# Kernel tuning notes

Hardware: AMD Instinct MI355X
Metric: run time of the kernel (lower is better)

Reference implementation:

```python
import jax, jax.numpy as jnp
import numpy as np


def setup_inputs() -> dict:
    key = jax.random.key(0)
    k_x, k_b = jax.random.split(key)
    B, C, H, W = 32, 512, 32, 32
    x = jax.random.normal(k_x, (B, C, H, W), dtype=jnp.float32)
    beta = jax.random.normal(k_b, (1,), dtype=jnp.float32)
    return {"x": x, "beta": beta}


def reference(x, beta):
    B, C, H, W = x.shape
    feat = x.reshape(B, C, H * W)                       # [B, C, N]
    # channel-channel Gram matrix: [B, C, C]
    attn = jnp.einsum('bcn,bdn->bcd', feat, feat)
    # DANet-style reversed scores: rowmax - score, then softmax over last dim
    attn = jnp.max(attn, axis=-1, keepdims=True) - attn
    attn = jax.nn.softmax(attn, axis=-1)
    feat_e = jnp.einsum('bcd,bdn->bcn', attn, feat).reshape(B, C, H, W)
    return beta * feat_e + x
```

## Files before the change

### kernel.cpp

```cpp
#include <hip/hip_runtime.h>
#include <math.h>

constexpr int B = 32, C = 512, N = 1024;

typedef float f32x4 __attribute__((ext_vector_type(4)));
typedef _Float16 f16x8 __attribute__((ext_vector_type(8)));
typedef unsigned short u16x4 __attribute__((ext_vector_type(4)));
typedef unsigned short u16x8 __attribute__((ext_vector_type(8)));

__device__ __forceinline__ unsigned short f32_to_f16u(float v) {
  union { _Float16 h; unsigned short u; } cv; cv.h = (_Float16)v; return cv.u;
}
__device__ __forceinline__ float f16u_to_f32(unsigned short u) {
  union { _Float16 h; unsigned short u; } cv; cv.u = u; return (float)cv.h;
}

__device__ __forceinline__ void glds16(const void* g, void* l) {
  __builtin_amdgcn_global_load_lds((const __attribute__((address_space(1))) void*)g,
                                   (__attribute__((address_space(3))) void*)l, 16, 0, 0);
}

__global__ __launch_bounds__(256) void convert_kernel(const float* __restrict__ x,
                                                      unsigned short* __restrict__ xf,
                                                      unsigned short* __restrict__ xfT) {
  const int b = blockIdx.z;
  const int cy = blockIdx.y * 64;
  const int nx = blockIdx.x * 64;
  const int t = threadIdx.x;
  const int r = t >> 4, c4 = (t & 15) * 4;

  __shared__ unsigned T[64][65];

#pragma unroll
  for (int rr = 0; rr < 64; rr += 16) {
    const int row = rr + r;
    const size_t gi = ((size_t)b * C + cy + row) * N + nx + c4;
    const float4 v = *(const float4*)&x[gi];
    u16x4 h;
    h[0] = f32_to_f16u(v.x); h[1] = f32_to_f16u(v.y);
    h[2] = f32_to_f16u(v.z); h[3] = f32_to_f16u(v.w);
    *(u16x4*)&xf[gi] = h;
    T[row][c4 + 0] = h[0]; T[row][c4 + 1] = h[1];
    T[row][c4 + 2] = h[2]; T[row][c4 + 3] = h[3];
  }
  __syncthreads();
#pragma unroll
  for (int rr = 0; rr < 64; rr += 16) {
    const int nrow = rr + r;
    u16x4 o;
    o[0] = (unsigned short)T[c4 + 0][nrow]; o[1] = (unsigned short)T[c4 + 1][nrow];
    o[2] = (unsigned short)T[c4 + 2][nrow]; o[3] = (unsigned short)T[c4 + 3][nrow];
    *(u16x4*)&xfT[((size_t)b * N + nx + nrow) * C + cy + c4] = o;
  }
}

__global__ __launch_bounds__(512, 2) void gram_soft_av(const unsigned short* __restrict__ xf,
                                                       const unsigned short* __restrict__ xfT,
                                                       const float* __restrict__ beta,
                                                       float* __restrict__ out) {
  const int l = blockIdx.x;
  const int xcd = l & 7, seq = l >> 3;
  const int b = xcd + 8 * (seq >> 3);
  const int i0 = (seq & 7) * 64;

  const unsigned short* __restrict__ Fh = xf  + (size_t)b * C * N;
  const unsigned short* __restrict__ FT = xfT + (size_t)b * N * C;
  float* __restrict__ ob = out + (size_t)b * C * N;

  __shared__ __align__(16) unsigned short Pb[4][512 * 32];
  unsigned short* Atile = &Pb[2][0];

  const int t = threadIdx.x, wave = t >> 6, lane = t & 63;
  const int lrow = lane & 15, quad = lane >> 4;
  const int srow = lane >> 2;
  const int sel  = ((lane & 3) ^ ((lane >> 3) & 3)) * 8;

  f32x4 acc[4][4] = {};

#define STAGE1(k0, nb)                                                    \
  {                                                                       \
    _Pragma("unroll")                                                     \
    for (int cc = 0; cc < 4; ++cc) {                                      \
      const int chunk = wave * 4 + cc;                                    \
      const int row = chunk * 16 + srow;                                  \
      glds16(Fh + (size_t)row * N + (k0) + sel, &Pb[nb][chunk * 512]);    \
    }                                                                     \
  }

#define LOADFRAG1(AH, BH, jj)                                             \
  {                                                                       \
    const unsigned short* __restrict__ Pc = Pb[(jj) & 3];                 \
    _Pragma("unroll")                                                     \
    for (int ti = 0; ti < 4; ++ti) {                                      \
      const int r = i0 + ti * 16 + lrow;                                  \
      AH[ti] = *(const f16x8*)&Pc[r * 32 + (quad ^ ((r >> 1) & 3)) * 8];  \
    }                                                                     \
    _Pragma("unroll")                                                     \
    for (int tj = 0; tj < 4; ++tj) {                                      \
      const int r = wave * 64 + tj * 16 + lrow;                           \
      BH[tj] = *(const f16x8*)&Pc[r * 32 + (quad ^ ((r >> 1) & 3)) * 8];  \
    }                                                                     \
  }

#define MFMA16(AH, BH, ACC)                                               \
  {                                                                       \
    __builtin_amdgcn_s_setprio(1);                                        \
    _Pragma("unroll")                                                     \
    for (int ti = 0; ti < 4; ++ti)                                        \
      _Pragma("unroll")                                                   \
      for (int tj = 0; tj < 4; ++tj)                                      \
        ACC[ti][tj] = __builtin_amdgcn_mfma_f32_16x16x32_f16(AH[ti], BH[tj], ACC[ti][tj], 0, 0, 0); \
    __builtin_amdgcn_s_setprio(0);                                        \
  }

#define P1BODY(CA, CB, NA, NB, j)                                         \
  {                                                                       \
    if ((j) < 29)       asm volatile("s_waitcnt vmcnt(8) lgkmcnt(0)" ::: "memory"); \
    else if ((j) == 29) asm volatile("s_waitcnt vmcnt(4) lgkmcnt(0)" ::: "memory"); \
    else                asm volatile("s_waitcnt vmcnt(0) lgkmcnt(0)" ::: "memory"); \
    __builtin_amdgcn_s_barrier();                                         \
    if ((j) + 4 < 32) STAGE1(((j) + 4) * 32, ((j) + 4) & 3);              \
    if ((j) + 1 < 32) LOADFRAG1(NA, NB, (j) + 1);                         \
    MFMA16(CA, CB, acc);                                                  \
  }

  STAGE1(0, 0);
  STAGE1(32, 1);
  STAGE1(64, 2);
  STAGE1(96, 3);
  asm volatile("s_waitcnt vmcnt(12)" ::: "memory");
  __builtin_amdgcn_s_barrier();

  f16x8 a0h[4], b0h[4], a1h[4], b1h[4];
  LOADFRAG1(a0h, b0h, 0);

  for (int j = 0; j < 32; j += 2) {
    P1BODY(a0h, b0h, a1h, b1h, j);
    P1BODY(a1h, b1h, a0h, b0h, j + 1);
  }
#undef P1BODY
#undef STAGE1

  __syncthreads();
  float* red = (float*)&Pb[0][0];
  float* fin = red + 512;

  float m[16];
#pragma unroll
  for (int ti = 0; ti < 4; ++ti)
#pragma unroll
    for (int rr = 0; rr < 4; ++rr)
      m[ti * 4 + rr] = fminf(fminf(acc[ti][0][rr], acc[ti][1][rr]),
                             fminf(acc[ti][2][rr], acc[ti][3][rr]));
#pragma unroll
  for (int o = 1; o < 16; o <<= 1)
#pragma unroll
    for (int s = 0; s < 16; ++s) m[s] = fminf(m[s], __shfl_xor(m[s], o, 64));
  if (lrow == 0)
#pragma unroll
    for (int ti = 0; ti < 4; ++ti)
#pragma unroll
      for (int rr = 0; rr < 4; ++rr)
        red[wave * 64 + ti * 16 + quad * 4 + rr] = m[ti * 4 + rr];
  __syncthreads();
  if (t < 64) {
    float v = red[t];
#pragma unroll
    for (int j = 1; j < 8; ++j) v = fminf(v, red[j * 64 + t]);
    fin[t] = v;
  }
  __syncthreads();

  float sm[16];
#pragma unroll
  for (int ti = 0; ti < 4; ++ti)
#pragma unroll
    for (int rr = 0; rr < 4; ++rr) {
      const float mn = fin[ti * 16 + quad * 4 + rr];
      float s = 0.f;
#pragma unroll
      for (int tj = 0; tj < 4; ++tj) {
        const float e = __expf(mn - acc[ti][tj][rr]);
        acc[ti][tj][rr] = e;
        s += e;
      }
      sm[ti * 4 + rr] = s;
    }
#pragma unroll
  for (int o = 1; o < 16; o <<= 1)
#pragma unroll
    for (int s = 0; s < 16; ++s) sm[s] += __shfl_xor(sm[s], o, 64);
  if (lrow == 0)
#pragma unroll
    for (int ti = 0; ti < 4; ++ti)
#pragma unroll
      for (int rr = 0; rr < 4; ++rr)
        red[wave * 64 + ti * 16 + quad * 4 + rr] = sm[ti * 4 + rr];
  __syncthreads();
  if (t < 64) {
    float v = 0.f;
#pragma unroll
    for (int j = 0; j < 8; ++j) v += red[j * 64 + t];
    fin[t] = 1.0f / v;
  }
  __syncthreads();

#pragma unroll
  for (int ti = 0; ti < 4; ++ti)
#pragma unroll
    for (int rr = 0; rr < 4; ++rr) {
      const float inv = fin[ti * 16 + quad * 4 + rr];
      const int rl = ti * 16 + quad * 4 + rr;
#pragma unroll
      for (int tj = 0; tj < 4; ++tj) {
        const int gcol = wave * 64 + tj * 16 + lrow;
        Atile[rl * 512 + ((((gcol >> 3) ^ (rl & 7)) << 3) | (gcol & 7))] =
            f32_to_f16u(acc[ti][tj][rr] * inv);
      }
    }
  __syncthreads();

  const float bv = beta[0];

  for (int jp = 0; jp < 2; ++jp) {
    f32x4 eacc[4][4] = {};
    u16x8 rsA[4];
#define LOADR_E(k0)                                                            \
    {                                                                          \
      _Pragma("unroll")                                                        \
      for (int cc = 0; cc < 4; ++cc) {                                         \
        const int chunk = wave * 4 + cc;                                       \
        const int row = chunk * 16 + srow;                                     \
        rsA[cc] = *(const u16x8*)&FT[(size_t)(jp * 512 + row) * C + (k0) + sel]; \
      }                                                                        \
    }
#define WRITER_E(nb)                                                           \
    {                                                                          \
      _Pragma("unroll")                                                        \
      for (int cc = 0; cc < 4; ++cc) {                                         \
        const int chunk = wave * 4 + cc;                                       \
        *(u16x8*)&Pb[nb][chunk * 512 + lane * 8] = rsA[cc];                    \
      }                                                                        \
    }
#define LOADFRAG2(AH, BH, uu)                                                  \
    {                                                                          \
      const unsigned short* __restrict__ Pc = Pb[(uu) & 1];                    \
      const int kk = (uu) * 32;                                                \
      _Pragma("unroll")                                                        \
      for (int ti = 0; ti < 4; ++ti) {                                         \
        const int ra = ti * 16 + lrow;                                         \
        AH[ti] = *(const f16x8*)&Atile[ra * 512 + ((((kk >> 3) + quad) ^ (ra & 7)) << 3)]; \
      }                                                                        \
      _Pragma("unroll")                                                        \
      for (int tj = 0; tj < 4; ++tj) {                                         \
        const int rb = wave * 64 + tj * 16 + lrow;                             \
        BH[tj] = *(const f16x8*)&Pc[rb * 32 + ((quad ^ ((rb >> 1) & 3)) << 3)]; \
      }                                                                        \
    }
#define P2BODY(CA, CB, NA, NB, u)                                              \
    {                                                                          \
      if ((u) + 1 < 16) WRITER_E(((u) + 1) & 1);                               \
      if ((u) + 2 < 16) LOADR_E(((u) + 2) * 32);                               \
      asm volatile("s_waitcnt lgkmcnt(0)" ::: "memory");                       \
      __builtin_amdgcn_s_barrier();                                            \
      if ((u) + 1 < 16) LOADFRAG2(NA, NB, (u) + 1);                            \
      MFMA16(CA, CB, eacc);                                                    \
    }

    LOADR_E(0);
    WRITER_E(0);
    LOADR_E(32);
    asm volatile("s_waitcnt lgkmcnt(0)" ::: "memory");
    __builtin_amdgcn_s_barrier();
    LOADFRAG2(a0h, b0h, 0);

    for (int u = 0; u < 16; u += 2) {
      P2BODY(a0h, b0h, a1h, b1h, u);
      P2BODY(a1h, b1h, a0h, b0h, u + 1);
    }
#undef P2BODY
#undef LOADFRAG2
#undef LOADR_E
#undef WRITER_E

    float* fs = (float*)&Pb[0][0] + wave * 1024;
#pragma unroll
    for (int ti = 0; ti < 4; ++ti) {
#pragma unroll
      for (int tj = 0; tj < 4; ++tj)
#pragma unroll
        for (int r = 0; r < 4; ++r)
          fs[(quad * 4 + r) * 64 + tj * 16 + lrow] = eacc[ti][tj][r];
      asm volatile("s_waitcnt lgkmcnt(0)" ::: "memory");
#pragma unroll
      for (int p = 0; p < 4; ++p) {
        const int f = p * 64 + lane;
        const int rr2 = f >> 4, cc4 = (f & 15) * 4;
        const f32x4 e = *(const f32x4*)&fs[rr2 * 64 + cc4];
        const int gr = i0 + ti * 16 + rr2;
        const int gc = jp * 512 + wave * 64 + cc4;
        const size_t o = (size_t)gr * N + gc;
        const u16x4 xv = *(const u16x4*)&Fh[o];
        f32x4 ov;
        ov[0] = fmaf(bv, e[0], f16u_to_f32(xv[0]));
        ov[1] = fmaf(bv, e[1], f16u_to_f32(xv[1]));
        ov[2] = fmaf(bv, e[2], f16u_to_f32(xv[2]));
        ov[3] = fmaf(bv, e[3], f16u_to_f32(xv[3]));
        __builtin_nontemporal_store(ov, (f32x4*)&ob[o]);
      }
      asm volatile("s_waitcnt lgkmcnt(0)" ::: "memory");
    }
  }
#undef MFMA16
#undef LOADFRAG1
}

extern "C" void kernel_launch(void* const* d_in, const int* in_sizes, int n_in,
                              void* d_out, int out_size, void* d_ws, size_t ws_size,
                              hipStream_t stream) {
  const float* x    = (const float*)d_in[0];
  const float* beta = (const float*)d_in[1];
  float* out = (float*)d_out;

  char* ws = (char*)d_ws;
  unsigned short* xf  = (unsigned short*)ws; ws += (size_t)B * C * N * 2;
  unsigned short* xfT = (unsigned short*)ws;

  convert_kernel<<<dim3(N / 64, C / 64, B), dim3(256), 0, stream>>>(x, xf, xfT);
  gram_soft_av  <<<dim3(256),               dim3(512), 0, stream>>>(xf, xfT, beta, out);
}
```

Baseline: 171.0 us.

## Load MFMA operands directly from global memory instead of LDS staging

Drops the LDS-staged, barrier-synchronised pipelines in both the Gram and attention-times-V phases. Each wave now loads its f16 fragments straight from global memory (xf and xfT) into registers, double-buffering them in registers across MFMA steps. This removes barriers, LDS traffic and the async global-to-LDS copies, but it issues redundant global loads across waves and uncoalesced 16-byte row reads, leaning on L2/L1 instead of shared memory. The LDS buffers are split into separate static arrays as a side effect.

```diff
diff --git a/kernel.cpp b/kernel.cpp
--- a/kernel.cpp
+++ b/kernel.cpp
@@ -6,18 +6,12 @@
 typedef float f32x4 __attribute__((ext_vector_type(4)));
 typedef _Float16 f16x8 __attribute__((ext_vector_type(8)));
 typedef unsigned short u16x4 __attribute__((ext_vector_type(4)));
-typedef unsigned short u16x8 __attribute__((ext_vector_type(8)));
 
 __device__ __forceinline__ unsigned short f32_to_f16u(float v) {
   union { _Float16 h; unsigned short u; } cv; cv.h = (_Float16)v; return cv.u;
 }
 __device__ __forceinline__ float f16u_to_f32(unsigned short u) {
   union { _Float16 h; unsigned short u; } cv; cv.u = u; return (float)cv.h;
-}
-
-__device__ __forceinline__ void glds16(const void* g, void* l) {
-  __builtin_amdgcn_global_load_lds((const __attribute__((address_space(1))) void*)g,
-                                   (__attribute__((address_space(3))) void*)l, 16, 0, 0);
 }
 
 __global__ __launch_bounds__(256) void convert_kernel(const float* __restrict__ x,
@@ -59,48 +53,23 @@
                                                        const float* __restrict__ beta,
                                                        float* __restrict__ out) {
   const int l = blockIdx.x;
-  const int xcd = l & 7, seq = l >> 3;
-  const int b = xcd + 8 * (seq >> 3);
+  const int seq = l >> 3;
+  const int b = (l & 7) + 8 * (seq >> 3);
   const int i0 = (seq & 7) * 64;
 
   const unsigned short* __restrict__ Fh = xf  + (size_t)b * C * N;
   const unsigned short* __restrict__ FT = xfT + (size_t)b * N * C;
   float* __restrict__ ob = out + (size_t)b * C * N;
 
-  __shared__ __align__(16) unsigned short Pb[4][512 * 32];
-  unsigned short* Atile = &Pb[2][0];
+  __shared__ __align__(16) unsigned short Atile[64 * 512];
+  __shared__ float red[512];
+  __shared__ float fin[64];
+  __shared__ __align__(16) float fsA[8][1024];
 
   const int t = threadIdx.x, wave = t >> 6, lane = t & 63;
   const int lrow = lane & 15, quad = lane >> 4;
-  const int srow = lane >> 2;
-  const int sel  = ((lane & 3) ^ ((lane >> 3) & 3)) * 8;
 
   f32x4 acc[4][4] = {};
-
-#define STAGE1(k0, nb)                                                    \
-  {                                                                       \
-    _Pragma("unroll")                                                     \
-    for (int cc = 0; cc < 4; ++cc) {                                      \
-      const int chunk = wave * 4 + cc;                                    \
-      const int row = chunk * 16 + srow;                                  \
-      glds16(Fh + (size_t)row * N + (k0) + sel, &Pb[nb][chunk * 512]);    \
-    }                                                                     \
-  }
-
-#define LOADFRAG1(AH, BH, jj)                                             \
-  {                                                                       \
-    const unsigned short* __restrict__ Pc = Pb[(jj) & 3];                 \
-    _Pragma("unroll")                                                     \
-    for (int ti = 0; ti < 4; ++ti) {                                      \
-      const int r = i0 + ti * 16 + lrow;                                  \
-      AH[ti] = *(const f16x8*)&Pc[r * 32 + (quad ^ ((r >> 1) & 3)) * 8];  \
-    }                                                                     \
-    _Pragma("unroll")                                                     \
-    for (int tj = 0; tj < 4; ++tj) {                                      \
-      const int r = wave * 64 + tj * 16 + lrow;                           \
-      BH[tj] = *(const f16x8*)&Pc[r * 32 + (quad ^ ((r >> 1) & 3)) * 8];  \
-    }                                                                     \
-  }
 
 #define MFMA16(AH, BH, ACC)                                               \
   {                                                                       \
@@ -113,37 +82,27 @@
     __builtin_amdgcn_s_setprio(0);                                        \
   }
 
-#define P1BODY(CA, CB, NA, NB, j)                                         \
+#define LDG1(AH, BH, j)                                                   \
   {                                                                       \
-    if ((j) < 29)       asm volatile("s_waitcnt vmcnt(8) lgkmcnt(0)" ::: "memory"); \
-    else if ((j) == 29) asm volatile("s_waitcnt vmcnt(4) lgkmcnt(0)" ::: "memory"); \
-    else                asm volatile("s_waitcnt vmcnt(0) lgkmcnt(0)" ::: "memory"); \
-    __builtin_amdgcn_s_barrier();                                         \
-    if ((j) + 4 < 32) STAGE1(((j) + 4) * 32, ((j) + 4) & 3);              \
-    if ((j) + 1 < 32) LOADFRAG1(NA, NB, (j) + 1);                         \
-    MFMA16(CA, CB, acc);                                                  \
-  }
-
-  STAGE1(0, 0);
-  STAGE1(32, 1);
-  STAGE1(64, 2);
-  STAGE1(96, 3);
-  asm volatile("s_waitcnt vmcnt(12)" ::: "memory");
-  __builtin_amdgcn_s_barrier();
-
-  f16x8 a0h[4], b0h[4], a1h[4], b1h[4];
-  LOADFRAG1(a0h, b0h, 0);
-
+    const int k0 = (j) * 32 + quad * 8;                                   \
+    _Pragma("unroll")                                                     \
+    for (int ti = 0; ti < 4; ++ti)                                        \
+      AH[ti] = *(const f16x8*)&Fh[(size_t)(i0 + ti * 16 + lrow) * N + k0];\
+    _Pragma("unroll")                                                     \
+    for (int tj = 0; tj < 4; ++tj)                                        \
+      BH[tj] = *(const f16x8*)&Fh[(size_t)(wave * 64 + tj * 16 + lrow) * N + k0]; \
+  }
+
+  f16x8 a0[4], b0[4], a1[4], b1[4];
+  LDG1(a0, b0, 0);
+  LDG1(a1, b1, 1);
   for (int j = 0; j < 32; j += 2) {
-    P1BODY(a0h, b0h, a1h, b1h, j);
-    P1BODY(a1h, b1h, a0h, b0h, j + 1);
-  }
-#undef P1BODY
-#undef STAGE1
-
-  __syncthreads();
-  float* red = (float*)&Pb[0][0];
-  float* fin = red + 512;
+    MFMA16(a0, b0, acc);
+    if (j + 2 < 32) LDG1(a0, b0, j + 2);
+    MFMA16(a1, b1, acc);
+    if (j + 3 < 32) LDG1(a1, b1, j + 3);
+  }
+#undef LDG1
 
   float m[16];
 #pragma unroll
@@ -224,66 +183,30 @@
 
   for (int jp = 0; jp < 2; ++jp) {
     f32x4 eacc[4][4] = {};
-    u16x8 rsA[4];
-#define LOADR_E(k0)                                                            \
+#define LDG2(AH, BH, u)                                                        \
     {                                                                          \
-      _Pragma("unroll")                                                        \
-      for (int cc = 0; cc < 4; ++cc) {                                         \
-        const int chunk = wave * 4 + cc;                                       \
-        const int row = chunk * 16 + srow;                                     \
-        rsA[cc] = *(const u16x8*)&FT[(size_t)(jp * 512 + row) * C + (k0) + sel]; \
-      }                                                                        \
-    }
-#define WRITER_E(nb)                                                           \
-    {                                                                          \
-      _Pragma("unroll")                                                        \
-      for (int cc = 0; cc < 4; ++cc) {                                         \
-        const int chunk = wave * 4 + cc;                                       \
-        *(u16x8*)&Pb[nb][chunk * 512 + lane * 8] = rsA[cc];                    \
-      }                                                                        \
-    }
-#define LOADFRAG2(AH, BH, uu)                                                  \
-    {                                                                          \
-      const unsigned short* __restrict__ Pc = Pb[(uu) & 1];                    \
-      const int kk = (uu) * 32;                                                \
+      const int kk = (u) * 32;                                                 \
       _Pragma("unroll")                                                        \
       for (int ti = 0; ti < 4; ++ti) {                                         \
         const int ra = ti * 16 + lrow;                                         \
         AH[ti] = *(const f16x8*)&Atile[ra * 512 + ((((kk >> 3) + quad) ^ (ra & 7)) << 3)]; \
       }                                                                        \
       _Pragma("unroll")                                                        \
-      for (int tj = 0; tj < 4; ++tj) {                                         \
-        const int rb = wave * 64 + tj * 16 + lrow;                             \
-        BH[tj] = *(const f16x8*)&Pc[rb * 32 + ((quad ^ ((rb >> 1) & 3)) << 3)]; \
-      }                                                                        \
-    }
-#define P2BODY(CA, CB, NA, NB, u)                                              \
-    {                                                                          \
-      if ((u) + 1 < 16) WRITER_E(((u) + 1) & 1);                               \
-      if ((u) + 2 < 16) LOADR_E(((u) + 2) * 32);                               \
-      asm volatile("s_waitcnt lgkmcnt(0)" ::: "memory");                       \
-      __builtin_amdgcn_s_barrier();                                            \
-      if ((u) + 1 < 16) LOADFRAG2(NA, NB, (u) + 1);                            \
-      MFMA16(CA, CB, eacc);                                                    \
-    }
-
-    LOADR_E(0);
-    WRITER_E(0);
-    LOADR_E(32);
-    asm volatile("s_waitcnt lgkmcnt(0)" ::: "memory");
-    __builtin_amdgcn_s_barrier();
-    LOADFRAG2(a0h, b0h, 0);
-
+      for (int tj = 0; tj < 4; ++tj)                                           \
+        BH[tj] = *(const f16x8*)&FT[(size_t)(jp * 512 + wave * 64 + tj * 16 + lrow) * C + kk + quad * 8]; \
+    }
+
+    LDG2(a0, b0, 0);
+    LDG2(a1, b1, 1);
     for (int u = 0; u < 16; u += 2) {
-      P2BODY(a0h, b0h, a1h, b1h, u);
-      P2BODY(a1h, b1h, a0h, b0h, u + 1);
-    }
-#undef P2BODY
-#undef LOADFRAG2
-#undef LOADR_E
-#undef WRITER_E
-
-    float* fs = (float*)&Pb[0][0] + wave * 1024;
+      MFMA16(a0, b0, eacc);
+      if (u + 2 < 16) LDG2(a0, b0, u + 2);
+      MFMA16(a1, b1, eacc);
+      if (u + 3 < 16) LDG2(a1, b1, u + 3);
+    }
+#undef LDG2
+
+    float* fs = &fsA[wave][0];
 #pragma unroll
     for (int ti = 0; ti < 4; ++ti) {
 #pragma unroll
@@ -312,7 +235,6 @@
     }
   }
 #undef MFMA16
-#undef LOADFRAG1
 }
 
 extern "C" void kernel_launch(void* const* d_in, const int* in_sizes, int n_in,
```

New measurement: 211.9 us. 24.0% more time.
